# Optimization experiments

Hardware: AMD Instinct MI355X
Metric: run time of the kernel (lower is better)

Reference implementation:

```python
import jax, jax.numpy as jnp
import numpy as np

N_NODES = 100000
N_EDGES = 1600000
D = 64        # atom_embed_dim
EF = 4        # edge_feat_dim
V = 100       # num_elements


def setup_inputs() -> dict:
    key = jax.random.key(0)
    ks = jax.random.split(key, 10)
    x_ids = jax.random.randint(ks[0], (N_NODES,), 0, V, dtype=jnp.int64 if jax.config.jax_enable_x64 else jnp.int32)
    edge_index = jax.random.randint(ks[1], (2, N_EDGES), 0, N_NODES, dtype=jnp.int64 if jax.config.jax_enable_x64 else jnp.int32)
    edge_attr = jax.random.normal(ks[2], (N_EDGES, EF), dtype=jnp.float32)
    emb = jax.random.normal(ks[3], (V, D), dtype=jnp.float32)
    s_in = 1.0 / np.sqrt(D + EF)
    s_d = 1.0 / np.sqrt(D)
    W1 = jax.random.uniform(ks[4], (D, D + EF), jnp.float32, -s_in, s_in)
    b1 = jax.random.uniform(ks[5], (D,), jnp.float32, -s_in, s_in)
    Wu1 = jax.random.uniform(ks[6], (D, D), jnp.float32, -s_d, s_d)
    bu1 = jax.random.uniform(ks[7], (D,), jnp.float32, -s_d, s_d)
    W2 = jax.random.uniform(ks[8], (D, D + EF), jnp.float32, -s_in, s_in)
    b2 = jax.random.uniform(ks[9], (D,), jnp.float32, -s_in, s_in)
    k2 = jax.random.split(jax.random.key(1), 2)
    Wu2 = jax.random.uniform(k2[0], (D, D), jnp.float32, -s_d, s_d)
    bu2 = jax.random.uniform(k2[1], (D,), jnp.float32, -s_d, s_d)
    return {"x_ids": x_ids, "edge_index": edge_index, "edge_attr": edge_attr,
            "emb": emb, "W1": W1, "b1": b1, "Wu1": Wu1, "bu1": bu1,
            "W2": W2, "b2": b2, "Wu2": Wu2, "bu2": bu2}


def _round(x, src, dst, edge_attr, Wm, bm, Wu, bu):
    # gather src node feats, concat edge feats, msg MLP, scatter-add to dst
    m = jnp.concatenate([x[src], edge_attr], axis=-1)       # (E, D+EF)
    m = jax.nn.relu(m @ Wm.T + bm)                           # (E, D)
    agg = jax.ops.segment_sum(m, dst, num_segments=x.shape[0])  # (N, D)
    return jax.nn.relu((x + agg) @ Wu.T + bu)                # (N, D)


def reference(x_ids, edge_index, edge_attr, emb, W1, b1, Wu1, bu1, W2, b2, Wu2, bu2):
    src, dst = edge_index[0], edge_index[1]
    x = emb[x_ids]                                           # (N, D)
    x = _round(x, src, dst, edge_attr, W1, b1, Wu1, bu1)
    x = _round(x, src, dst, edge_attr, W2, b2, Wu2, bu2)
    return x.mean(axis=0)                                    # (D,)
```

## Files before the change

### kernel.cpp

```cpp
#include <hip/hip_runtime.h>

#define DD    64
#define WCOLS 68
#define VV    100

struct alignas(32) Rec {
    float4 ea;
    int    src;
    int    voc;
    int    p0, p1;
};

__device__ __forceinline__ float lane_bcast(float v, int k) {
    return __int_as_float(__builtin_amdgcn_readlane(__float_as_int(v), k));
}

__global__ __launch_bounds__(256) void hist_kernel(
    const int* __restrict__ dst, int* __restrict__ deg, int E)
{
    int i = blockIdx.x * 256 + threadIdx.x;
    int stride = gridDim.x * 256;
    for (; i < E; i += stride) atomicAdd(&deg[dst[i]], 1);
}

__global__ __launch_bounds__(256) void scan1_kernel(
    const int* __restrict__ deg, int* __restrict__ rowp, int* __restrict__ bsum, int N)
{
    __shared__ int lds[256];
    int base = blockIdx.x * 1024;
    int t = threadIdx.x;
    int idx0 = base + t * 4;
    int v[4];
    #pragma unroll
    for (int j = 0; j < 4; ++j) v[j] = (idx0 + j < N) ? deg[idx0 + j] : 0;
    lds[t] = v[0] + v[1] + v[2] + v[3];
    __syncthreads();
    for (int off = 1; off < 256; off <<= 1) {
        int x = (t >= off) ? lds[t - off] : 0;
        __syncthreads();
        lds[t] += x;
        __syncthreads();
    }
    int run = (t > 0) ? lds[t - 1] : 0;
    if (t == 255) bsum[blockIdx.x] = lds[255];
    #pragma unroll
    for (int j = 0; j < 4; ++j) {
        if (idx0 + j < N) rowp[idx0 + j] = run;
        run += v[j];
    }
}

__global__ __launch_bounds__(256) void scan2_kernel(int* __restrict__ bsum, int nchunks)
{
    __shared__ int lds[256];
    int t = threadIdx.x;
    int v = (t < nchunks) ? bsum[t] : 0;
    lds[t] = v;
    __syncthreads();
    for (int off = 1; off < 256; off <<= 1) {
        int x = (t >= off) ? lds[t - off] : 0;
        __syncthreads();
        lds[t] += x;
        __syncthreads();
    }
    if (t < nchunks) bsum[t] = (t > 0) ? lds[t - 1] : 0;
}

__global__ __launch_bounds__(256) void scan3_kernel(
    int* __restrict__ rowp, const int* __restrict__ bsum, int* __restrict__ cursor,
    int N, int E)
{
    int i = blockIdx.x * 256 + threadIdx.x;
    if (i == 0) rowp[N] = E;
    if (i < N) {
        int v = rowp[i] + bsum[i >> 10];
        rowp[i] = v;
        cursor[i] = v;
    }
}

__global__ __launch_bounds__(256) void fill_kernel(
    const int* __restrict__ src, const int* __restrict__ dst,
    const int* __restrict__ x_ids, const float* __restrict__ eattr,
    int* __restrict__ cursor, Rec* __restrict__ rec, int E)
{
    int i = blockIdx.x * 256 + threadIdx.x;
    int stride = gridDim.x * 256;
    for (; i < E; i += stride) {
        int s = src[i];
        int d = dst[i];
        int pos = atomicAdd(&cursor[d], 1);
        Rec r;
        r.ea  = *(const float4*)(eattr + (size_t)i * 4);
        r.src = s;
        r.voc = x_ids[s];
        r.p0 = 0; r.p1 = 0;
        rec[pos] = r;
    }
}

__global__ __launch_bounds__(256) void vocab_kernel(
    const float* __restrict__ emb, const float* __restrict__ W1,
    const float* __restrict__ b1, float* __restrict__ YV)
{
    __shared__ float WaT[64 * 64];
    for (int i = threadIdx.x; i < 64 * 64; i += 256) {
        int d = i & 63, k = i >> 6;
        WaT[i] = W1[d * WCOLS + k];
    }
    __syncthreads();

    int lane = threadIdx.x & 63;
    int wv = blockIdx.x * 4 + (threadIdx.x >> 6);
    if (wv >= VV) return;
    float xv = emb[wv * DD + lane];
    float acc = b1[lane];
    #pragma unroll 8
    for (int k = 0; k < 64; ++k)
        acc = fmaf(WaT[k * 64 + lane], lane_bcast(xv, k), acc);
    YV[wv * DD + lane] = acc;
}

__global__ __launch_bounds__(256) void round1_kernel(
    const int* __restrict__ rowp, const Rec* __restrict__ rec,
    const float* __restrict__ YV,
    const int* __restrict__ x_ids, const float* __restrict__ emb,
    const float* __restrict__ W1,
    const float* __restrict__ Wu, const float* __restrict__ bu,
    float* __restrict__ x1, int N)
{
    __shared__ float YVs[VV * 64];
    __shared__ float WuT[64 * 64];
    for (int i = threadIdx.x; i < VV * 64; i += 256) YVs[i] = YV[i];
    for (int i = threadIdx.x; i < 64 * 64; i += 256) {
        int d = i & 63, k = i >> 6;
        WuT[i] = Wu[d * DD + k];
    }
    __syncthreads();

    int lane = threadIdx.x & 63;
    int wid  = __builtin_amdgcn_readfirstlane((blockIdx.x * 256 + (int)threadIdx.x) >> 6);
    int nw   = (gridDim.x * 256) >> 6;
    float w0 = W1[lane * WCOLS + 64];
    float w1 = W1[lane * WCOLS + 65];
    float w2 = W1[lane * WCOLS + 66];
    float w3 = W1[lane * WCOLS + 67];
    float biasu = bu[lane];

    for (int n = wid; n < N; n += nw) {
        int beg = rowp[n], end = rowp[n + 1];
        float acc = 0.f;
        int e = beg;
        for (; e + 7 < end; e += 8) {
            int   v8[8]; float4 a8[8];
            #pragma unroll
            for (int j = 0; j < 8; ++j) { v8[j] = rec[e + j].voc; a8[j] = rec[e + j].ea; }
            float y8[8];
            #pragma unroll
            for (int j = 0; j < 8; ++j) y8[j] = YVs[v8[j] * 64 + lane];
            #pragma unroll
            for (int j = 0; j < 8; ++j) {
                float m = fmaf(w0, a8[j].x, y8[j]);
                m = fmaf(w1, a8[j].y, m);
                m = fmaf(w2, a8[j].z, m);
                m = fmaf(w3, a8[j].w, m);
                acc += fmaxf(m, 0.f);
            }
        }
        for (; e < end; ++e) {
            int v0 = rec[e].voc;
            float4 a0 = rec[e].ea;
            float m0 = fmaf(w0, a0.x, YVs[v0 * 64 + lane]);
            m0 = fmaf(w1, a0.y, m0);
            m0 = fmaf(w2, a0.z, m0);
            m0 = fmaf(w3, a0.w, m0);
            acc += fmaxf(m0, 0.f);
        }

        int id = x_ids[n];
        float v = emb[(size_t)id * DD + lane] + acc;
        float au = biasu;
        #pragma unroll 8
        for (int k = 0; k < 64; ++k)
            au = fmaf(WuT[k * 64 + lane], lane_bcast(v, k), au);
        x1[(size_t)n * DD + lane] = fmaxf(au, 0.f);
    }
}

__global__ __launch_bounds__(256) void yb_kernel(
    const float* __restrict__ x1, const float* __restrict__ Wn,
    const float* __restrict__ bn, float* __restrict__ Yb, int N)
{
    __shared__ float WnT[64 * 64];
    for (int i = threadIdx.x; i < 64 * 64; i += 256) {
        int d = i & 63, k = i >> 6;
        WnT[i] = Wn[d * WCOLS + k];
    }
    __syncthreads();

    int lane = threadIdx.x & 63;
    int wid  = (blockIdx.x * 256 + threadIdx.x) >> 6;
    int nw   = (gridDim.x * 256) >> 6;
    float bias = bn[lane];

    for (int base = wid * 4; base < N; base += nw * 4) {
        int nvalid = N - base; if (nvalid > 4) nvalid = 4;
        float xv[4], acc[4];
        #pragma unroll
        for (int j = 0; j < 4; ++j) {
            xv[j] = (j < nvalid) ? x1[(size_t)(base + j) * DD + lane] : 0.f;
            acc[j] = bias;
        }
        #pragma unroll 8
        for (int k = 0; k < 64; ++k) {
            float w = WnT[k * 64 + lane];
            #pragma unroll
            for (int j = 0; j < 4; ++j)
                acc[j] = fmaf(w, lane_bcast(xv[j], k), acc[j]);
        }
        #pragma unroll
        for (int j = 0; j < 4; ++j)
            if (j < nvalid) Yb[(size_t)(base + j) * DD + lane] = acc[j];
    }
}

__global__ __launch_bounds__(256) void round2_kernel(
    const int* __restrict__ rowp, const Rec* __restrict__ rec,
    const float* __restrict__ Y_in, const float* __restrict__ Wm,
    const float* __restrict__ Wu, const float* __restrict__ bu,
    const float* __restrict__ x1, float* __restrict__ out_mean,
    int N, float inv_n)
{
    __shared__ float WuT[64 * 64];
    __shared__ float red[256];
    for (int i = threadIdx.x; i < 64 * 64; i += 256) {
        int d = i & 63, k = i >> 6;
        WuT[i] = Wu[d * DD + k];
    }
    __syncthreads();

    int lane = threadIdx.x & 63;
    int wid  = __builtin_amdgcn_readfirstlane((blockIdx.x * 256 + (int)threadIdx.x) >> 6);
    int nw   = (gridDim.x * 256) >> 6;
    float w0 = Wm[lane * WCOLS + 64];
    float w1 = Wm[lane * WCOLS + 65];
    float w2 = Wm[lane * WCOLS + 66];
    float w3 = Wm[lane * WCOLS + 67];
    float biasu = bu[lane];
    float lsum = 0.f;

    for (int n = wid; n < N; n += nw) {
        int beg = rowp[n], end = rowp[n + 1];
        float acc = 0.f;
        int e = beg;
        for (; e + 3 < end; e += 4) {
            int s0 = rec[e].src, s1 = rec[e + 1].src, s2 = rec[e + 2].src, s3 = rec[e + 3].src;
            float4 a0 = rec[e].ea, a1 = rec[e + 1].ea, a2 = rec[e + 2].ea, a3 = rec[e + 3].ea;
            float y0 = Y_in[(size_t)s0 * DD + lane];
            float y1 = Y_in[(size_t)s1 * DD + lane];
            float y2 = Y_in[(size_t)s2 * DD + lane];
            float y3 = Y_in[(size_t)s3 * DD + lane];
            float m0 = y0 + w0 * a0.x + w1 * a0.y + w2 * a0.z + w3 * a0.w;
            float m1 = y1 + w0 * a1.x + w1 * a1.y + w2 * a1.z + w3 * a1.w;
            float m2 = y2 + w0 * a2.x + w1 * a2.y + w2 * a2.z + w3 * a2.w;
            float m3 = y3 + w0 * a3.x + w1 * a3.y + w2 * a3.z + w3 * a3.w;
            acc += fmaxf(m0, 0.f) + fmaxf(m1, 0.f) + fmaxf(m2, 0.f) + fmaxf(m3, 0.f);
        }
        for (; e < end; ++e) {
            int s0 = rec[e].src;
            float4 a0 = rec[e].ea;
            float y0 = Y_in[(size_t)s0 * DD + lane];
            float m0 = y0 + w0 * a0.x + w1 * a0.y + w2 * a0.z + w3 * a0.w;
            acc += fmaxf(m0, 0.f);
        }

        size_t o = (size_t)n * DD + lane;
        float v = x1[o] + acc;
        float au = biasu;
        #pragma unroll 8
        for (int k = 0; k < 64; ++k)
            au = fmaf(WuT[k * 64 + lane], lane_bcast(v, k), au);
        lsum += fmaxf(au, 0.f);
    }

    red[threadIdx.x] = lsum;
    __syncthreads();
    if (threadIdx.x < 64) {
        float s = red[threadIdx.x] + red[threadIdx.x + 64] +
                  red[threadIdx.x + 128] + red[threadIdx.x + 192];
        unsafeAtomicAdd(&out_mean[threadIdx.x], s * inv_n);
    }
}

extern "C" void kernel_launch(void* const* d_in, const int* in_sizes, int n_in,
                              void* d_out, int out_size, void* d_ws, size_t ws_size,
                              hipStream_t stream) {
    const int*   x_ids = (const int*)d_in[0];
    const int*   ei    = (const int*)d_in[1];
    const float* eattr = (const float*)d_in[2];
    const float* emb   = (const float*)d_in[3];
    const float* W1    = (const float*)d_in[4];
    const float* b1    = (const float*)d_in[5];
    const float* Wu1   = (const float*)d_in[6];
    const float* bu1   = (const float*)d_in[7];
    const float* W2    = (const float*)d_in[8];
    const float* b2    = (const float*)d_in[9];
    const float* Wu2   = (const float*)d_in[10];
    const float* bu2   = (const float*)d_in[11];

    const int N = in_sizes[0];
    const int E = in_sizes[1] / 2;
    const int* src = ei;
    const int* dst = ei + E;

    float* ws = (float*)d_ws;
    size_t stride = (size_t)N * DD;
    float*  x1   = ws;
    float*  Yb   = ws + stride;
    Rec*    rec  = (Rec*)(ws + 2 * stride);
    int*    rowp = (int*)(rec + E);
    int*    deg  = rowp + N + 1;
    int*    cur  = deg + N;
    int*    bsum = cur + N;
    float*  YV   = (float*)(bsum + 256);

    float* out = (float*)d_out;
    float inv_n = 1.0f / (float)N;
    int nchunks = (N + 1023) / 1024;

    hipMemsetAsync(deg, 0, (size_t)N * sizeof(int), stream);
    hipMemsetAsync(out, 0, DD * sizeof(float), stream);

    hist_kernel <<<2048, 256, 0, stream>>>(dst, deg, E);
    scan1_kernel<<<nchunks, 256, 0, stream>>>(deg, rowp, bsum, N);
    scan2_kernel<<<1, 256, 0, stream>>>(bsum, nchunks);
    scan3_kernel<<<(N + 255) / 256, 256, 0, stream>>>(rowp, bsum, cur, N, E);
    fill_kernel <<<2048, 256, 0, stream>>>(src, dst, x_ids, eattr, cur, rec, E);

    vocab_kernel<<<(VV + 3) / 4, 256, 0, stream>>>(emb, W1, b1, YV);

    round1_kernel<<<2048, 256, 0, stream>>>(
        rowp, rec, YV, x_ids, emb, W1, Wu1, bu1, x1, N);
    yb_kernel<<<1024, 256, 0, stream>>>(x1, W2, b2, Yb, N);
    round2_kernel<<<2048, 256, 0, stream>>>(
        rowp, rec, Yb, W2, Wu2, bu2, x1, out, N, inv_n);
}
```

Before: 592.4 us.

## Split round-1 node update out of edge kernel and fuse it with Yb projection

The round-1 edge aggregation kernel now only writes the aggregated messages, dropping its 64x64 Wu matmul and the WuT shared-memory load. A new node kernel reads the aggregate plus the embedding, applies the Wu update for four nodes per wave, then immediately applies the round-2 message projection W2 and writes both x1 and Yb. This spreads the Wu weight reads over four nodes and lightens the edge kernel's LDS use, which may let more waves run at once. The cost is an extra write and read of an N x 64 intermediate through x1.

```diff
diff --git a/kernel.cpp b/kernel.cpp
--- a/kernel.cpp
+++ b/kernel.cpp
@@ -121,21 +121,13 @@
     YV[wv * DD + lane] = acc;
 }
 
-__global__ __launch_bounds__(256) void round1_kernel(
+__global__ __launch_bounds__(256) void edge_r1_kernel(
     const int* __restrict__ rowp, const Rec* __restrict__ rec,
-    const float* __restrict__ YV,
-    const int* __restrict__ x_ids, const float* __restrict__ emb,
-    const float* __restrict__ W1,
-    const float* __restrict__ Wu, const float* __restrict__ bu,
-    float* __restrict__ x1, int N)
+    const float* __restrict__ YV, const float* __restrict__ W1,
+    float* __restrict__ agg, int N)
 {
     __shared__ float YVs[VV * 64];
-    __shared__ float WuT[64 * 64];
     for (int i = threadIdx.x; i < VV * 64; i += 256) YVs[i] = YV[i];
-    for (int i = threadIdx.x; i < 64 * 64; i += 256) {
-        int d = i & 63, k = i >> 6;
-        WuT[i] = Wu[d * DD + k];
-    }
     __syncthreads();
 
     int lane = threadIdx.x & 63;
@@ -145,7 +137,6 @@
     float w1 = W1[lane * WCOLS + 65];
     float w2 = W1[lane * WCOLS + 66];
     float w3 = W1[lane * WCOLS + 67];
-    float biasu = bu[lane];
 
     for (int n = wid; n < N; n += nw) {
         int beg = rowp[n], end = rowp[n + 1];
@@ -176,24 +167,21 @@
             m0 = fmaf(w3, a0.w, m0);
             acc += fmaxf(m0, 0.f);
         }
-
-        int id = x_ids[n];
-        float v = emb[(size_t)id * DD + lane] + acc;
-        float au = biasu;
-        #pragma unroll 8
-        for (int k = 0; k < 64; ++k)
-            au = fmaf(WuT[k * 64 + lane], lane_bcast(v, k), au);
-        x1[(size_t)n * DD + lane] = fmaxf(au, 0.f);
-    }
-}
-
-__global__ __launch_bounds__(256) void yb_kernel(
-    const float* __restrict__ x1, const float* __restrict__ Wn,
-    const float* __restrict__ bn, float* __restrict__ Yb, int N)
-{
+        agg[(size_t)n * DD + lane] = acc;
+    }
+}
+
+__global__ __launch_bounds__(256) void node1_kernel(
+    const int* __restrict__ x_ids, const float* __restrict__ emb,
+    const float* __restrict__ Wu, const float* __restrict__ bu,
+    const float* __restrict__ Wn, const float* __restrict__ bn,
+    float* __restrict__ x1 , float* __restrict__ Yb, int N)
+{
+    __shared__ float WuT[64 * 64];
     __shared__ float WnT[64 * 64];
     for (int i = threadIdx.x; i < 64 * 64; i += 256) {
         int d = i & 63, k = i >> 6;
+        WuT[i] = Wu[d * DD + k];
         WnT[i] = Wn[d * WCOLS + k];
     }
     __syncthreads();
@@ -201,26 +189,49 @@
     int lane = threadIdx.x & 63;
     int wid  = (blockIdx.x * 256 + threadIdx.x) >> 6;
     int nw   = (gridDim.x * 256) >> 6;
-    float bias = bn[lane];
+    float biasu = bu[lane];
+    float biasn = bn[lane];
 
     for (int base = wid * 4; base < N; base += nw * 4) {
         int nvalid = N - base; if (nvalid > 4) nvalid = 4;
-        float xv[4], acc[4];
+        float v[4], acc[4];
         #pragma unroll
         for (int j = 0; j < 4; ++j) {
-            xv[j] = (j < nvalid) ? x1[(size_t)(base + j) * DD + lane] : 0.f;
-            acc[j] = bias;
-        }
+            if (j < nvalid) {
+                size_t o = (size_t)(base + j) * DD + lane;
+                v[j] = emb[(size_t)x_ids[base + j] * DD + lane] + x1[o];
+            } else v[j] = 0.f;
+            acc[j] = biasu;
+        }
+        #pragma unroll 8
+        for (int k = 0; k < 64; ++k) {
+            float w = WuT[k * 64 + lane];
+            #pragma unroll
+            for (int j = 0; j < 4; ++j)
+                acc[j] = fmaf(w, lane_bcast(v[j], k), acc[j]);
+        }
+        float o4[4];
+        #pragma unroll
+        for (int j = 0; j < 4; ++j) o4[j] = fmaxf(acc[j], 0.f);
+
+        float acc2[4];
+        #pragma unroll
+        for (int j = 0; j < 4; ++j) acc2[j] = biasn;
         #pragma unroll 8
         for (int k = 0; k < 64; ++k) {
             float w = WnT[k * 64 + lane];
             #pragma unroll
             for (int j = 0; j < 4; ++j)
-                acc[j] = fmaf(w, lane_bcast(xv[j], k), acc[j]);
+                acc2[j] = fmaf(w, lane_bcast(o4[j], k), acc2[j]);
         }
         #pragma unroll
-        for (int j = 0; j < 4; ++j)
-            if (j < nvalid) Yb[(size_t)(base + j) * DD + lane] = acc[j];
+        for (int j = 0; j < 4; ++j) {
+            if (j < nvalid) {
+                size_t o = (size_t)(base + j) * DD + lane;
+                x1[o] = o4[j];
+                Yb[o] = acc2[j];
+            }
+        }
     }
 }
 
@@ -339,9 +350,8 @@
 
     vocab_kernel<<<(VV + 3) / 4, 256, 0, stream>>>(emb, W1, b1, YV);
 
-    round1_kernel<<<2048, 256, 0, stream>>>(
-        rowp, rec, YV, x_ids, emb, W1, Wu1, bu1, x1, N);
-    yb_kernel<<<1024, 256, 0, stream>>>(x1, W2, b2, Yb, N);
+    edge_r1_kernel<<<2048, 256, 0, stream>>>(rowp, rec, YV, W1, x1, N);
+    node1_kernel<<<1024, 256, 0, stream>>>(x_ids, emb, Wu1, bu1, W2, b2, x1, Yb, N);
     round2_kernel<<<2048, 256, 0, stream>>>(
         rowp, rec, Yb, W2, Wu2, bu2, x1, out, N, inv_n);
 }
```

Result: faster. 562.8 us (-5.0%).
